# Kernel tuning notes

Hardware: AMD Instinct MI355X
Metric: run time of the kernel (lower is better)

Reference implementation:

```python
import jax, jax.numpy as jnp
import numpy as np

NUM_HEADS = 16

def _rope(t, cos, sin):
    # t: [B,H,T,hd]; cos/sin: [T,half]
    half = t.shape[-1] // 2
    t1, t2 = t[..., :half], t[..., half:]
    return jnp.concatenate((t1 * cos - t2 * sin, t1 * sin + t2 * cos), axis=-1)

def setup_inputs() -> dict:
    key = jax.random.key(0)
    ks = jax.random.split(key, 5)
    B, T, D = 2, 2048, 2048
    s = 0.02
    return {
        'x': jax.random.normal(ks[0], (B, T, D), jnp.float32),
        'w_qkv': jax.random.normal(ks[1], (3 * D, D), jnp.float32) * s,
        'b_qkv': jax.random.normal(ks[2], (3 * D,), jnp.float32) * s,
        'w_out': jax.random.normal(ks[3], (D, D), jnp.float32) * s,
        'b_out': jax.random.normal(ks[4], (D,), jnp.float32) * s,
    }

def reference(x, w_qkv, b_qkv, w_out, b_out):
    B, T, D = x.shape
    H = NUM_HEADS
    hd = D // H
    half = hd // 2
    # fused QKV projection (torch Linear: x @ W^T + b)
    qkv = (x @ w_qkv.T + b_qkv).reshape(B, T, H, 3, hd)
    q, k, v = qkv[..., 0, :], qkv[..., 1, :], qkv[..., 2, :]
    q, k, v = (jnp.transpose(t, (0, 2, 1, 3)) for t in (q, k, v))  # [B,H,T,hd]
    # RoPE frequencies (buffer computed as in __init__)
    theta = 1.0 / (10000.0 ** (jnp.arange(half, dtype=jnp.float32) / half))
    freq = jnp.arange(T, dtype=jnp.float32)[:, None] * theta[None, :]  # [T,half]
    cos, sin = jnp.cos(freq), jnp.sin(freq)
    q = _rope(q, cos, sin)
    k = _rope(k, cos, sin)
    # causal attention; NOTE: source scales by embed_dim**-0.5
    scale = D ** (-0.5)
    scores = jnp.einsum('bhqd,bhkd->bhqk', q, k) * scale
    mask = jnp.triu(jnp.full((T, T), -1e9, dtype=scores.dtype), k=1)
    weights = jax.nn.softmax(scores + mask, axis=-1)
    attn = jnp.einsum('bhqk,bhkd->bhqd', weights, v)
    attn = jnp.transpose(attn, (0, 2, 1, 3)).reshape(B, T, D)
    return attn @ w_out.T + b_out
```

## Files before the change

### kernel.cpp

```cpp
#include <hip/hip_runtime.h>
#include <math.h>

#define NHEAD 16
#define TSEQ  2048
#define BATCH 2
#define DM    2048

typedef __attribute__((ext_vector_type(8))) short bf16x8;
typedef __attribute__((ext_vector_type(4))) float f32x4;

__device__ __forceinline__ short f2bf(float f) {
    unsigned u = __builtin_bit_cast(unsigned, f);
    u += 0x7fff + ((u >> 16) & 1);
    return (short)(u >> 16);
}
__device__ __forceinline__ float bf2f(short s) {
    unsigned u = ((unsigned)(unsigned short)s) << 16;
    return __builtin_bit_cast(float, u);
}
__device__ __forceinline__ void gload_lds16(const void* g, void* l) {
    __builtin_amdgcn_global_load_lds(
        (const __attribute__((address_space(1))) unsigned int*)g,
        (__attribute__((address_space(3))) unsigned int*)l, 16, 0, 0);
}

__global__ __launch_bounds__(256)
void cast_all(const float* __restrict__ x, short* __restrict__ xb,
              const float* __restrict__ wq, short* __restrict__ wqb,
              const float* __restrict__ wo, short* __restrict__ wob)
{
    int bid = blockIdx.x;
    const float* src; short* dst; int lb;
    if (bid < 4096)       { src = x;  dst = xb;  lb = bid; }
    else if (bid < 10240) { src = wq; dst = wqb; lb = bid - 4096; }
    else                  { src = wo; dst = wob; lb = bid - 10240; }
    int i = (lb * 256 + threadIdx.x) * 8;
    float4 a = *(const float4*)(src + i);
    float4 b = *(const float4*)(src + i + 4);
    bf16x8 o;
    o[0]=f2bf(a.x); o[1]=f2bf(a.y); o[2]=f2bf(a.z); o[3]=f2bf(a.w);
    o[4]=f2bf(b.x); o[5]=f2bf(b.y); o[6]=f2bf(b.z); o[7]=f2bf(b.w);
    *(bf16x8*)(dst + i) = o;
}

__global__ __launch_bounds__(256)
void gemm_qkv_rope(const short* __restrict__ A, const short* __restrict__ W,
                   const float* __restrict__ bias, short* __restrict__ qfrag,
                   short* __restrict__ kfrag, short* __restrict__ vfrag)
{
    const int K = 2048;
    __shared__ short sm[17408];
    short* As = sm;
    short* Bs = sm + 8192;
    const int tid = threadIdx.x;
    const int lane = tid & 63, w = tid >> 6;
    const int lane15 = lane & 15, quad = lane >> 4;
    const int wr = w >> 1, wc = w & 1;
    const int row0 = blockIdx.y * 128, col0 = blockIdx.x * 128;

    f32x4 acc[4][4];
    #pragma unroll
    for (int mi = 0; mi < 4; ++mi)
        #pragma unroll
        for (int ni = 0; ni < 4; ++ni)
            acc[mi][ni] = (f32x4){0.f, 0.f, 0.f, 0.f};

    for (int kt = 0; kt < K; kt += 64) {
        __syncthreads();
        #pragma unroll
        for (int i = 0; i < 4; ++i) {
            int ci = i * 256 + tid;
            int row = ci >> 3, lc = ci & 7;
            int gc = lc ^ (row & 7);
            gload_lds16(A + (size_t)(row0 + row) * K + kt + gc * 8, As + ci * 8);
            gload_lds16(W + (size_t)(col0 + row) * K + kt + gc * 8, Bs + ci * 8);
        }
        __syncthreads();
        #pragma unroll
        for (int kc = 0; kc < 2; ++kc) {
            bf16x8 af[4], bfr[4];
            #pragma unroll
            for (int mi = 0; mi < 4; ++mi) {
                int r = wr * 64 + mi * 16 + lane15;
                af[mi] = *(const bf16x8*)(As + r * 64 + ((kc * 4 + quad) ^ (r & 7)) * 8);
            }
            #pragma unroll
            for (int ni = 0; ni < 4; ++ni) {
                int r = wc * 64 + ni * 16 + lane15;
                bfr[ni] = *(const bf16x8*)(Bs + r * 64 + ((kc * 4 + quad) ^ (r & 7)) * 8);
            }
            #pragma unroll
            for (int mi = 0; mi < 4; ++mi)
                #pragma unroll
                for (int ni = 0; ni < 4; ++ni)
                    acc[mi][ni] = __builtin_amdgcn_mfma_f32_16x16x32_bf16(
                        af[mi], bfr[ni], acc[mi][ni], 0, 0, 0);
        }
    }

    const int head = col0 / 384;
    const int type = (col0 % 384) >> 7;
    const int b    = row0 >> 11;
    const int t0g  = row0 & 2047;
    const int bh   = b * NHEAD + head;

    __syncthreads();
    #pragma unroll
    for (int ni = 0; ni < 4; ++ni) {
        int d = wc * 64 + ni * 16 + lane15;
        float bv = bias[col0 + d];
        #pragma unroll
        for (int mi = 0; mi < 4; ++mi) {
            int rowb = wr * 64 + mi * 16 + quad * 4;
            #pragma unroll
            for (int r = 0; r < 4; ++r)
                sm[(rowb + r) * 136 + d] = f2bf(acc[mi][ni][r] + bv);
        }
    }
    __syncthreads();

    if (type < 2) {
        const float sc = (type == 0) ? 0.022097086912079608f : 1.0f;
        short* dst = (type == 0 ? qfrag : kfrag) + (size_t)bh * 262144;
        #pragma unroll
        for (int it = 0; it < 4; ++it) {
            int c = it * 256 + tid;
            int l15 = c & 15, q_ = (c >> 4) & 3, kc = (c >> 6) & 1, rowhi = c >> 7;
            int lrow = rowhi * 16 + l15;
            int t = t0g + lrow;
            bf16x8 a8 = *(const bf16x8*)(sm + lrow * 136 + kc * 32 + q_ * 8);
            bf16x8 b8 = *(const bf16x8*)(sm + lrow * 136 + kc * 32 + q_ * 8 + 64);
            bf16x8 oa, ob;
            #pragma unroll
            for (int j = 0; j < 8; ++j) {
                int d = kc * 32 + q_ * 8 + j;
                float trev = exp2f(-(float)d * (13.287712379549449f / 64.0f))
                             * 0.15915494309189535f;
                float ang = (float)t * trev;
                float fr = ang - floorf(ang);
                float sn, cs;
                __sincosf(fr * 6.283185307179586f, &sn, &cs);
                float va = bf2f(a8[j]), vb = bf2f(b8[j]);
                oa[j] = f2bf((va * cs - vb * sn) * sc);
                ob[j] = f2bf((va * sn + vb * cs) * sc);
            }
            size_t base = (size_t)((t0g >> 4) + rowhi) * 2048 + (q_ * 16 + l15) * 8;
            *(bf16x8*)(dst + base + kc * 512)        = oa;
            *(bf16x8*)(dst + base + kc * 512 + 1024) = ob;
        }
    } else {
        short* dst = vfrag + (size_t)bh * 262144;
        #pragma unroll
        for (int it = 0; it < 8; ++it) {
            int c = it * 256 + tid;
            int lane_ = c & 63, rest = c >> 6;
            int q_ = lane_ >> 4, l15 = lane_ & 15;
            int dt = rest & 7, kc2 = (rest >> 3) & 1, kbt = rest >> 4;
            int d = dt * 16 + l15;
            bf16x8 v;
            #pragma unroll
            for (int j = 0; j < 8; ++j)
                v[j] = sm[(kbt * 64 + kc2 * 32 + q_ * 8 + j) * 136 + d];
            *(bf16x8*)(dst + (size_t)((t0g >> 6) + kbt) * 8192
                        + dt * 1024 + kc2 * 512 + lane_ * 8) = v;
        }
    }
}

__global__ __launch_bounds__(256)
void gemm_out(const short* __restrict__ A, const short* __restrict__ W,
              const float* __restrict__ bias, float* __restrict__ Cout,
              int N, int K)
{
    __shared__ short As[128 * 64];
    __shared__ short Bs[128 * 64];
    const int tid = threadIdx.x;
    const int lane = tid & 63, w = tid >> 6;
    const int lane15 = lane & 15, quad = lane >> 4;
    const int wr = w >> 1, wc = w & 1;
    const int row0 = blockIdx.y * 128, col0 = blockIdx.x * 128;

    f32x4 acc[4][4];
    #pragma unroll
    for (int mi = 0; mi < 4; ++mi)
        #pragma unroll
        for (int ni = 0; ni < 4; ++ni)
            acc[mi][ni] = (f32x4){0.f, 0.f, 0.f, 0.f};

    for (int kt = 0; kt < K; kt += 64) {
        __syncthreads();
        #pragma unroll
        for (int i = 0; i < 4; ++i) {
            int ci = i * 256 + tid;
            int row = ci >> 3, lc = ci & 7;
            int gc = lc ^ (row & 7);
            gload_lds16(A + (size_t)(row0 + row) * K + kt + gc * 8, As + ci * 8);
            gload_lds16(W + (size_t)(col0 + row) * K + kt + gc * 8, Bs + ci * 8);
        }
        __syncthreads();
        #pragma unroll
        for (int kc = 0; kc < 2; ++kc) {
            bf16x8 af[4], bfr[4];
            #pragma unroll
            for (int mi = 0; mi < 4; ++mi) {
                int r = wr * 64 + mi * 16 + lane15;
                af[mi] = *(const bf16x8*)(As + r * 64 + ((kc * 4 + quad) ^ (r & 7)) * 8);
            }
            #pragma unroll
            for (int ni = 0; ni < 4; ++ni) {
                int r = wc * 64 + ni * 16 + lane15;
                bfr[ni] = *(const bf16x8*)(Bs + r * 64 + ((kc * 4 + quad) ^ (r & 7)) * 8);
            }
            #pragma unroll
            for (int mi = 0; mi < 4; ++mi)
                #pragma unroll
                for (int ni = 0; ni < 4; ++ni)
                    acc[mi][ni] = __builtin_amdgcn_mfma_f32_16x16x32_bf16(
                        af[mi], bfr[ni], acc[mi][ni], 0, 0, 0);
        }
    }

    #pragma unroll
    for (int mi = 0; mi < 4; ++mi)
        #pragma unroll
        for (int ni = 0; ni < 4; ++ni) {
            int col = col0 + wc * 64 + ni * 16 + lane15;
            float bv = bias[col];
            #pragma unroll
            for (int r = 0; r < 4; ++r) {
                int row = row0 + wr * 64 + mi * 16 + quad * 4 + r;
                Cout[(size_t)row * N + col] = acc[mi][ni][r] + bv;
            }
        }
}

__global__ __launch_bounds__(256)
void attn3(const short* __restrict__ qfrag, const short* __restrict__ kfrag,
           const short* __restrict__ vfrag, short* __restrict__ attnb)
{
    __shared__ short KV[2][16384];
    __shared__ short Pb[4][1152];
    const int tid = threadIdx.x;
    const int lane = tid & 63, w = tid >> 6;
    const int lane15 = lane & 15, quad = lane >> 4;
    const int g = (blockIdx.x + blockIdx.y) & 15;
    const int qb = blockIdx.z ? (15 - g) : g;
    const int h = blockIdx.y, b = blockIdx.z;
    const int bh = b * NHEAD + h;
    const int q0 = qb * 128;
    short* Pw = Pb[w];

    bf16x8 qf[2][4];
    {
        const short* qp = qfrag + (size_t)bh * 262144
                        + (size_t)(qb * 8 + w * 2) * 2048 + lane * 8;
        #pragma unroll
        for (int nq = 0; nq < 2; ++nq)
            #pragma unroll
            for (int kc = 0; kc < 4; ++kc)
                qf[nq][kc] = *(const bf16x8*)(qp + nq * 2048 + kc * 512);
    }

    f32x4 acc[8][2];
    #pragma unroll
    for (int dt = 0; dt < 8; ++dt)
        #pragma unroll
        for (int nq = 0; nq < 2; ++nq)
            acc[dt][nq] = (f32x4){0.f, 0.f, 0.f, 0.f};
    float m_s[2] = {-3e38f, -3e38f}, l_s[2] = {0.f, 0.f};

    const short* kf_src = kfrag + (size_t)bh * 262144;
    const short* vf_src = vfrag + (size_t)bh * 262144;
    const int kb_max = 2 * qb + 1;
    const int qtop = q0 + w * 32 + 31;
    const int diag0 = (q0 + w * 32) >> 6;

    #pragma unroll
    for (int i = 0; i < 4; ++i) {
        int ci = i * 256 + tid;
        gload_lds16(kf_src + ci * 8, KV[0] + ci * 8);
        gload_lds16(vf_src + ci * 8, KV[0] + 8192 + ci * 8);
    }

    for (int kb = 0; kb <= kb_max; ++kb) {
        __syncthreads();
        if (kb < kb_max) {
            const short* ks = kf_src + (size_t)(kb + 1) * 8192;
            const short* vs = vf_src + (size_t)(kb + 1) * 8192;
            short* kd = KV[(kb + 1) & 1];
            #pragma unroll
            for (int i = 0; i < 4; ++i) {
                int ci = i * 256 + tid;
                gload_lds16(ks + ci * 8, kd + ci * 8);
                gload_lds16(vs + ci * 8, kd + 8192 + ci * 8);
            }
        }
        if (kb * 64 > qtop) continue;
        const short* Ks = KV[kb & 1];
        const short* Vs = Ks + 8192;

        f32x4 st[2][4];
        #pragma unroll
        for (int nq = 0; nq < 2; ++nq)
            #pragma unroll
            for (int mi = 0; mi < 4; ++mi)
                st[nq][mi] = (f32x4){0.f, 0.f, 0.f, 0.f};
        #pragma unroll
        for (int mi = 0; mi < 4; ++mi) {
            bf16x8 kf4[4];
            #pragma unroll
            for (int kc = 0; kc < 4; ++kc)
                kf4[kc] = *(const bf16x8*)(Ks + ((mi * 4 + kc) * 64 + lane) * 8);
            #pragma unroll
            for (int kc = 0; kc < 4; ++kc)
                #pragma unroll
                for (int nq = 0; nq < 2; ++nq)
                    st[nq][mi] = __builtin_amdgcn_mfma_f32_16x16x32_bf16(
                        kf4[kc], qf[nq][kc], st[nq][mi], 0, 0, 0);
        }

        if (kb >= diag0) {
            #pragma unroll
            for (int nq = 0; nq < 2; ++nq) {
                int qg = q0 + w * 32 + nq * 16 + lane15;
                #pragma unroll
                for (int mi = 0; mi < 4; ++mi)
                    #pragma unroll
                    for (int r = 0; r < 4; ++r)
                        if (kb * 64 + mi * 16 + quad * 4 + r > qg)
                            st[nq][mi][r] = -3e38f;
            }
        }

        bf16x8 pb[2][2];
        #pragma unroll
        for (int nq = 0; nq < 2; ++nq) {
            float mt = st[nq][0][0];
            #pragma unroll
            for (int mi = 0; mi < 4; ++mi)
                #pragma unroll
                for (int r = 0; r < 4; ++r)
                    mt = fmaxf(mt, st[nq][mi][r]);
            mt = fmaxf(mt, __shfl_xor(mt, 16));
            mt = fmaxf(mt, __shfl_xor(mt, 32));
            float mn = fmaxf(m_s[nq], mt);
            float alpha = __expf(m_s[nq] - mn);
            m_s[nq] = mn;
            float sum = 0.f;
            #pragma unroll
            for (int mi = 0; mi < 4; ++mi)
                #pragma unroll
                for (int r = 0; r < 4; ++r) {
                    float p = __expf(st[nq][mi][r] - mn);
                    st[nq][mi][r] = p;
                    sum += p;
                }
            sum += __shfl_xor(sum, 16);
            sum += __shfl_xor(sum, 32);
            l_s[nq] = l_s[nq] * alpha + sum;
            #pragma unroll
            for (int dt = 0; dt < 8; ++dt) {
                acc[dt][nq][0] *= alpha; acc[dt][nq][1] *= alpha;
                acc[dt][nq][2] *= alpha; acc[dt][nq][3] *= alpha;
            }
            short* pr = Pw + lane15 * 72 + quad * 4;
            #pragma unroll
            for (int mi = 0; mi < 4; ++mi) {
                unsigned lo = (unsigned)(unsigned short)f2bf(st[nq][mi][0])
                            | ((unsigned)(unsigned short)f2bf(st[nq][mi][1]) << 16);
                unsigned hi = (unsigned)(unsigned short)f2bf(st[nq][mi][2])
                            | ((unsigned)(unsigned short)f2bf(st[nq][mi][3]) << 16);
                *(unsigned*)(pr + mi * 16)     = lo;
                *(unsigned*)(pr + mi * 16 + 2) = hi;
            }
            __asm__ volatile("s_waitcnt lgkmcnt(0)" ::: "memory");
            #pragma unroll
            for (int kc2 = 0; kc2 < 2; ++kc2)
                pb[nq][kc2] = *(const bf16x8*)(Pw + lane15 * 72 + kc2 * 32 + quad * 8);
            __asm__ volatile("s_waitcnt lgkmcnt(0)" ::: "memory");
        }

        #pragma unroll
        for (int dt = 0; dt < 8; ++dt)
            #pragma unroll
            for (int kc2 = 0; kc2 < 2; ++kc2) {
                bf16x8 vf = *(const bf16x8*)(Vs + ((dt * 2 + kc2) * 64 + lane) * 8);
                #pragma unroll
                for (int nq = 0; nq < 2; ++nq)
                    acc[dt][nq] = __builtin_amdgcn_mfma_f32_16x16x32_bf16(
                        vf, pb[nq][kc2], acc[dt][nq], 0, 0, 0);
            }
    }

    __syncthreads();
    short* Eb = KV[0];
    #pragma unroll
    for (int nq = 0; nq < 2; ++nq) {
        float inv = 1.f / l_s[nq];
        int qrow = w * 32 + nq * 16 + lane15;
        #pragma unroll
        for (int dt = 0; dt < 8; ++dt) {
            unsigned lo = (unsigned)(unsigned short)f2bf(acc[dt][nq][0] * inv)
                        | ((unsigned)(unsigned short)f2bf(acc[dt][nq][1] * inv) << 16);
            unsigned hi = (unsigned)(unsigned short)f2bf(acc[dt][nq][2] * inv)
                        | ((unsigned)(unsigned short)f2bf(acc[dt][nq][3] * inv) << 16);
            *(unsigned*)(Eb + qrow * 136 + dt * 16 + quad * 4)     = lo;
            *(unsigned*)(Eb + qrow * 136 + dt * 16 + quad * 4 + 2) = hi;
        }
    }
    __syncthreads();
    {
        int r = tid >> 1, half = tid & 1;
        short* orow = attnb + (size_t)(b * TSEQ + q0 + r) * DM + h * 128 + half * 64;
        #pragma unroll
        for (int i = 0; i < 8; ++i)
            *(bf16x8*)(orow + i * 8) =
                *(const bf16x8*)(Eb + r * 136 + half * 64 + i * 8);
    }
}

extern "C" void kernel_launch(void* const* d_in, const int* in_sizes, int n_in,
                              void* d_out, int out_size, void* d_ws, size_t ws_size,
                              hipStream_t stream)
{
    const float* x     = (const float*)d_in[0];
    const float* w_qkv = (const float*)d_in[1];
    const float* b_qkv = (const float*)d_in[2];
    const float* w_out = (const float*)d_in[3];
    const float* b_out = (const float*)d_in[4];
    float* out = (float*)d_out;

    char* ws = (char*)d_ws;
    short* xb    = (short*)(ws);
    short* wqkvb = (short*)(ws + 16777216);
    short* woutb = (short*)(ws + 41943040);
    short* qfrag = (short*)(ws + 50331648);
    short* kfrag = (short*)(ws + 67108864);
    short* vfrag = (short*)(ws + 83886080);
    short* attnb = xb;

    cast_all<<<12288, 256, 0, stream>>>(x, xb, w_qkv, wqkvb, w_out, woutb);

    {
        dim3 g2(48, 32);
        gemm_qkv_rope<<<g2, 256, 0, stream>>>(xb, wqkvb, b_qkv, qfrag, kfrag, vfrag);
    }
    {
        dim3 g2(16, NHEAD, BATCH);
        attn3<<<g2, 256, 0, stream>>>(qfrag, kfrag, vfrag, attnb);
    }
    {
        dim3 g2(16, 32);
        gemm_out<<<g2, 256, 0, stream>>>(attnb, woutb, b_out, out, 2048, 2048);
    }
}
```

Measured before the change: 381.0 us.

## Software-pipeline attention so next QK^T overlaps softmax/PV, use exp2 softmax

Restructures the attention main loop so the QK^T MFMAs for the next key block are issued right after the softmax of the current block and before its PV MFMAs. K/V DMA is moved to the end of each iteration with prefetch distance two over the double buffer. The Q scale now folds in log2(e), so softmax can use the hardware exp2 builtin instead of __expf, and the explicit lgkmcnt waits around the P round trip through LDS are dropped. The aim is to hide softmax latency behind matrix work, at the cost of more live registers (st and pbr held across phases) and an extra barrier per iteration.

```diff
diff --git a/kernel.cpp b/kernel.cpp
--- a/kernel.cpp
+++ b/kernel.cpp
@@ -120,7 +120,7 @@
     __syncthreads();
 
     if (type < 2) {
-        const float sc = (type == 0) ? 0.022097086912079608f : 1.0f;
+        const float sc = (type == 0) ? 0.031879357813f : 1.0f;
         short* dst = (type == 0 ? qfrag : kfrag) + (size_t)bh * 262144;
         #pragma unroll
         for (int it = 0; it < 4; ++it) {
@@ -235,7 +235,7 @@
 }
 
 __global__ __launch_bounds__(256)
-void attn3(const short* __restrict__ qfrag, const short* __restrict__ kfrag,
+void attn4(const short* __restrict__ qfrag, const short* __restrict__ kfrag,
            const short* __restrict__ vfrag, short* __restrict__ attnb)
 {
     __shared__ short KV[2][16384];
@@ -275,31 +275,19 @@
     const int qtop = q0 + w * 32 + 31;
     const int diag0 = (q0 + w * 32) >> 6;
 
-    #pragma unroll
-    for (int i = 0; i < 4; ++i) {
-        int ci = i * 256 + tid;
-        gload_lds16(kf_src + ci * 8, KV[0] + ci * 8);
-        gload_lds16(vf_src + ci * 8, KV[0] + 8192 + ci * 8);
-    }
-
-    for (int kb = 0; kb <= kb_max; ++kb) {
-        __syncthreads();
-        if (kb < kb_max) {
-            const short* ks = kf_src + (size_t)(kb + 1) * 8192;
-            const short* vs = vf_src + (size_t)(kb + 1) * 8192;
-            short* kd = KV[(kb + 1) & 1];
-            #pragma unroll
-            for (int i = 0; i < 4; ++i) {
-                int ci = i * 256 + tid;
-                gload_lds16(ks + ci * 8, kd + ci * 8);
-                gload_lds16(vs + ci * 8, kd + 8192 + ci * 8);
-            }
-        }
-        if (kb * 64 > qtop) continue;
-        const short* Ks = KV[kb & 1];
-        const short* Vs = Ks + 8192;
-
-        f32x4 st[2][4];
+    auto dma = [&](int kbn, short* dst) {
+        const short* ks = kf_src + (size_t)kbn * 8192;
+        const short* vs = vf_src + (size_t)kbn * 8192;
+        #pragma unroll
+        for (int i = 0; i < 4; ++i) {
+            int ci = i * 256 + tid;
+            gload_lds16(ks + ci * 8, dst + ci * 8);
+            gload_lds16(vs + ci * 8, dst + 8192 + ci * 8);
+        }
+    };
+
+    f32x4 st[2][4];
+    auto qk = [&](const short* Ks) {
         #pragma unroll
         for (int nq = 0; nq < 2; ++nq)
             #pragma unroll
@@ -318,78 +306,101 @@
                     st[nq][mi] = __builtin_amdgcn_mfma_f32_16x16x32_bf16(
                         kf4[kc], qf[nq][kc], st[nq][mi], 0, 0, 0);
         }
-
-        if (kb >= diag0) {
+    };
+
+    dma(0, KV[0]);
+    __syncthreads();
+    dma(1, KV[1]);
+    qk(KV[0]);
+
+    for (int kb = 0; kb <= kb_max; ++kb) {
+        const short* Vs = KV[kb & 1] + 8192;
+        const bool live = (kb * 64 <= qtop);
+        bf16x8 pbr[2][2];
+
+        if (live) {
+            if (kb >= diag0) {
+                #pragma unroll
+                for (int nq = 0; nq < 2; ++nq) {
+                    int qg = q0 + w * 32 + nq * 16 + lane15;
+                    #pragma unroll
+                    for (int mi = 0; mi < 4; ++mi)
+                        #pragma unroll
+                        for (int r = 0; r < 4; ++r)
+                            if (kb * 64 + mi * 16 + quad * 4 + r > qg)
+                                st[nq][mi][r] = -3e38f;
+                }
+            }
             #pragma unroll
             for (int nq = 0; nq < 2; ++nq) {
-                int qg = q0 + w * 32 + nq * 16 + lane15;
+                float mt = st[nq][0][0];
                 #pragma unroll
                 for (int mi = 0; mi < 4; ++mi)
                     #pragma unroll
                     for (int r = 0; r < 4; ++r)
-                        if (kb * 64 + mi * 16 + quad * 4 + r > qg)
-                            st[nq][mi][r] = -3e38f;
-            }
-        }
-
-        bf16x8 pb[2][2];
-        #pragma unroll
-        for (int nq = 0; nq < 2; ++nq) {
-            float mt = st[nq][0][0];
-            #pragma unroll
-            for (int mi = 0; mi < 4; ++mi)
-                #pragma unroll
-                for (int r = 0; r < 4; ++r)
-                    mt = fmaxf(mt, st[nq][mi][r]);
-            mt = fmaxf(mt, __shfl_xor(mt, 16));
-            mt = fmaxf(mt, __shfl_xor(mt, 32));
-            float mn = fmaxf(m_s[nq], mt);
-            float alpha = __expf(m_s[nq] - mn);
-            m_s[nq] = mn;
-            float sum = 0.f;
-            #pragma unroll
-            for (int mi = 0; mi < 4; ++mi)
-                #pragma unroll
-                for (int r = 0; r < 4; ++r) {
-                    float p = __expf(st[nq][mi][r] - mn);
-                    st[nq][mi][r] = p;
-                    sum += p;
+                        mt = fmaxf(mt, st[nq][mi][r]);
+                mt = fmaxf(mt, __shfl_xor(mt, 16));
+                mt = fmaxf(mt, __shfl_xor(mt, 32));
+                float mn = fmaxf(m_s[nq], mt);
+                float alpha = __builtin_amdgcn_exp2f(m_s[nq] - mn);
+                m_s[nq] = mn;
+                float sum = 0.f;
+                #pragma unroll
+                for (int mi = 0; mi < 4; ++mi)
+                    #pragma unroll
+                    for (int r = 0; r < 4; ++r) {
+                        float p = __builtin_amdgcn_exp2f(st[nq][mi][r] - mn);
+                        st[nq][mi][r] = p;
+                        sum += p;
+                    }
+                sum += __shfl_xor(sum, 16);
+                sum += __shfl_xor(sum, 32);
+                l_s[nq] = l_s[nq] * alpha + sum;
+                #pragma unroll
+                for (int dt = 0; dt < 8; ++dt) {
+                    acc[dt][nq][0] *= alpha; acc[dt][nq][1] *= alpha;
+                    acc[dt][nq][2] *= alpha; acc[dt][nq][3] *= alpha;
                 }
-            sum += __shfl_xor(sum, 16);
-            sum += __shfl_xor(sum, 32);
-            l_s[nq] = l_s[nq] * alpha + sum;
-            #pragma unroll
-            for (int dt = 0; dt < 8; ++dt) {
-                acc[dt][nq][0] *= alpha; acc[dt][nq][1] *= alpha;
-                acc[dt][nq][2] *= alpha; acc[dt][nq][3] *= alpha;
-            }
-            short* pr = Pw + lane15 * 72 + quad * 4;
-            #pragma unroll
-            for (int mi = 0; mi < 4; ++mi) {
-                unsigned lo = (unsigned)(unsigned short)f2bf(st[nq][mi][0])
-                            | ((unsigned)(unsigned short)f2bf(st[nq][mi][1]) << 16);
-                unsigned hi = (unsigned)(unsigned short)f2bf(st[nq][mi][2])
-                            | ((unsigned)(unsigned short)f2bf(st[nq][mi][3]) << 16);
-                *(unsigned*)(pr + mi * 16)     = lo;
-                *(unsigned*)(pr + mi * 16 + 2) = hi;
-            }
-            __asm__ volatile("s_waitcnt lgkmcnt(0)" ::: "memory");
-            #pragma unroll
-            for (int kc2 = 0; kc2 < 2; ++kc2)
-                pb[nq][kc2] = *(const bf16x8*)(Pw + lane15 * 72 + kc2 * 32 + quad * 8);
-            __asm__ volatile("s_waitcnt lgkmcnt(0)" ::: "memory");
-        }
-
-        #pragma unroll
-        for (int dt = 0; dt < 8; ++dt)
-            #pragma unroll
-            for (int kc2 = 0; kc2 < 2; ++kc2) {
-                bf16x8 vf = *(const bf16x8*)(Vs + ((dt * 2 + kc2) * 64 + lane) * 8);
-                #pragma unroll
-                for (int nq = 0; nq < 2; ++nq)
-                    acc[dt][nq] = __builtin_amdgcn_mfma_f32_16x16x32_bf16(
-                        vf, pb[nq][kc2], acc[dt][nq], 0, 0, 0);
-            }
+                short* pr = Pw + lane15 * 72 + quad * 4;
+                #pragma unroll
+                for (int mi = 0; mi < 4; ++mi) {
+                    unsigned lo = (unsigned)(unsigned short)f2bf(st[nq][mi][0])
+                                | ((unsigned)(unsigned short)f2bf(st[nq][mi][1]) << 16);
+                    unsigned hi = (unsigned)(unsigned short)f2bf(st[nq][mi][2])
+                                | ((unsigned)(unsigned short)f2bf(st[nq][mi][3]) << 16);
+                    *(unsigned*)(pr + mi * 16)     = lo;
+                    *(unsigned*)(pr + mi * 16 + 2) = hi;
+                }
+                #pragma unroll
+                for (int kc2 = 0; kc2 < 2; ++kc2)
+                    pbr[nq][kc2] = *(const bf16x8*)
+                        (Pw + lane15 * 72 + kc2 * 32 + quad * 8);
+            }
+        }
+
+        if (kb < kb_max) {
+            __syncthreads();
+            if ((kb + 1) * 64 <= qtop)
+                qk(KV[(kb + 1) & 1]);
+        }
+
+        if (live) {
+            #pragma unroll
+            for (int dt = 0; dt < 8; ++dt)
+                #pragma unroll
+                for (int kc2 = 0; kc2 < 2; ++kc2) {
+                    bf16x8 vf = *(const bf16x8*)(Vs + ((dt * 2 + kc2) * 64 + lane) * 8);
+                    #pragma unroll
+                    for (int nq = 0; nq < 2; ++nq)
+                        acc[dt][nq] = __builtin_amdgcn_mfma_f32_16x16x32_bf16(
+                            vf, pbr[nq][kc2], acc[dt][nq], 0, 0, 0);
+                }
+        }
+
+        if (kb + 2 <= kb_max) {
+            __syncthreads();
+            dma(kb + 2, KV[kb & 1]);
+        }
     }
 
     __syncthreads();
@@ -447,7 +458,7 @@
     }
     {
         dim3 g2(16, NHEAD, BATCH);
-        attn3<<<g2, 256, 0, stream>>>(qfrag, kfrag, vfrag, attnb);
+        attn4<<<g2, 256, 0, stream>>>(qfrag, kfrag, vfrag, attnb);
     }
     {
         dim3 g2(16, 32);
```

After: 454.8 us. 1.19x slower.

## Shrink attention query tile to 64 rows with single-buffered KV and exp2 softmax

Applied to the files above, without the earlier changes.

Rewrites the attention kernel to give each block 64 queries (16 per wave) instead of 128, which doubles the grid to 32x16x2 and removes the per-wave causal skip logic. K/V staging moves from a double-buffered prefetch to a single buffer loaded each iteration, so load latency is no longer overlapped with compute. The log2(e) factor is folded into the Q scale so softmax can use the native exp2. The P tile now goes through LDS with an XOR swizzle in place of padding. Occupancy rises from the smaller LDS and register footprint, but each K/V tile is reused by half as many queries and the loads are exposed.

```diff
diff --git a/kernel.cpp b/kernel.cpp
--- a/kernel.cpp
+++ b/kernel.cpp
@@ -120,7 +120,7 @@
     __syncthreads();
 
     if (type < 2) {
-        const float sc = (type == 0) ? 0.022097086912079608f : 1.0f;
+        const float sc = (type == 0) ? 0.031879357813f : 1.0f;
         short* dst = (type == 0 ? qfrag : kfrag) + (size_t)bh * 262144;
         #pragma unroll
         for (int it = 0; it < 4; ++it) {
@@ -235,76 +235,54 @@
 }
 
 __global__ __launch_bounds__(256)
-void attn3(const short* __restrict__ qfrag, const short* __restrict__ kfrag,
+void attn5(const short* __restrict__ qfrag, const short* __restrict__ kfrag,
            const short* __restrict__ vfrag, short* __restrict__ attnb)
 {
-    __shared__ short KV[2][16384];
-    __shared__ short Pb[4][1152];
+    __shared__ short KV[16384];
+    __shared__ short Pb[4][1024];
     const int tid = threadIdx.x;
     const int lane = tid & 63, w = tid >> 6;
     const int lane15 = lane & 15, quad = lane >> 4;
-    const int g = (blockIdx.x + blockIdx.y) & 15;
-    const int qb = blockIdx.z ? (15 - g) : g;
+    const int g = (blockIdx.x + blockIdx.y) & 31;
+    const int qb = blockIdx.z ? (31 - g) : g;
     const int h = blockIdx.y, b = blockIdx.z;
     const int bh = b * NHEAD + h;
-    const int q0 = qb * 128;
+    const int q0 = qb * 64;
     short* Pw = Pb[w];
-
-    bf16x8 qf[2][4];
+    short* Ks = KV;
+    short* Vs = KV + 8192;
+
+    bf16x8 qf[4];
     {
         const short* qp = qfrag + (size_t)bh * 262144
-                        + (size_t)(qb * 8 + w * 2) * 2048 + lane * 8;
-        #pragma unroll
-        for (int nq = 0; nq < 2; ++nq)
-            #pragma unroll
-            for (int kc = 0; kc < 4; ++kc)
-                qf[nq][kc] = *(const bf16x8*)(qp + nq * 2048 + kc * 512);
-    }
-
-    f32x4 acc[8][2];
+                        + (size_t)(qb * 4 + w) * 2048 + lane * 8;
+        #pragma unroll
+        for (int kc = 0; kc < 4; ++kc)
+            qf[kc] = *(const bf16x8*)(qp + kc * 512);
+    }
+
+    f32x4 acc[8];
     #pragma unroll
-    for (int dt = 0; dt < 8; ++dt)
-        #pragma unroll
-        for (int nq = 0; nq < 2; ++nq)
-            acc[dt][nq] = (f32x4){0.f, 0.f, 0.f, 0.f};
-    float m_s[2] = {-3e38f, -3e38f}, l_s[2] = {0.f, 0.f};
+    for (int dt = 0; dt < 8; ++dt) acc[dt] = (f32x4){0.f, 0.f, 0.f, 0.f};
+    float m_s = -3e38f, l_s = 0.f;
 
     const short* kf_src = kfrag + (size_t)bh * 262144;
     const short* vf_src = vfrag + (size_t)bh * 262144;
-    const int kb_max = 2 * qb + 1;
-    const int qtop = q0 + w * 32 + 31;
-    const int diag0 = (q0 + w * 32) >> 6;
-
-    #pragma unroll
-    for (int i = 0; i < 4; ++i) {
-        int ci = i * 256 + tid;
-        gload_lds16(kf_src + ci * 8, KV[0] + ci * 8);
-        gload_lds16(vf_src + ci * 8, KV[0] + 8192 + ci * 8);
-    }
-
-    for (int kb = 0; kb <= kb_max; ++kb) {
+    const int qg = q0 + w * 16 + lane15;
+
+    for (int kb = 0; kb <= qb; ++kb) {
+        if (kb) __syncthreads();
+        #pragma unroll
+        for (int i = 0; i < 4; ++i) {
+            int ci = i * 256 + tid;
+            gload_lds16(kf_src + (size_t)kb * 8192 + ci * 8, Ks + ci * 8);
+            gload_lds16(vf_src + (size_t)kb * 8192 + ci * 8, Vs + ci * 8);
+        }
         __syncthreads();
-        if (kb < kb_max) {
-            const short* ks = kf_src + (size_t)(kb + 1) * 8192;
-            const short* vs = vf_src + (size_t)(kb + 1) * 8192;
-            short* kd = KV[(kb + 1) & 1];
-            #pragma unroll
-            for (int i = 0; i < 4; ++i) {
-                int ci = i * 256 + tid;
-                gload_lds16(ks + ci * 8, kd + ci * 8);
-                gload_lds16(vs + ci * 8, kd + 8192 + ci * 8);
-            }
-        }
-        if (kb * 64 > qtop) continue;
-        const short* Ks = KV[kb & 1];
-        const short* Vs = Ks + 8192;
-
-        f32x4 st[2][4];
-        #pragma unroll
-        for (int nq = 0; nq < 2; ++nq)
-            #pragma unroll
-            for (int mi = 0; mi < 4; ++mi)
-                st[nq][mi] = (f32x4){0.f, 0.f, 0.f, 0.f};
+
+        f32x4 st[4];
+        #pragma unroll
+        for (int mi = 0; mi < 4; ++mi) st[mi] = (f32x4){0.f, 0.f, 0.f, 0.f};
         #pragma unroll
         for (int mi = 0; mi < 4; ++mi) {
             bf16x8 kf4[4];
@@ -313,109 +291,97 @@
                 kf4[kc] = *(const bf16x8*)(Ks + ((mi * 4 + kc) * 64 + lane) * 8);
             #pragma unroll
             for (int kc = 0; kc < 4; ++kc)
-                #pragma unroll
-                for (int nq = 0; nq < 2; ++nq)
-                    st[nq][mi] = __builtin_amdgcn_mfma_f32_16x16x32_bf16(
-                        kf4[kc], qf[nq][kc], st[nq][mi], 0, 0, 0);
-        }
-
-        if (kb >= diag0) {
-            #pragma unroll
-            for (int nq = 0; nq < 2; ++nq) {
-                int qg = q0 + w * 32 + nq * 16 + lane15;
-                #pragma unroll
-                for (int mi = 0; mi < 4; ++mi)
-                    #pragma unroll
-                    for (int r = 0; r < 4; ++r)
-                        if (kb * 64 + mi * 16 + quad * 4 + r > qg)
-                            st[nq][mi][r] = -3e38f;
-            }
-        }
-
-        bf16x8 pb[2][2];
-        #pragma unroll
-        for (int nq = 0; nq < 2; ++nq) {
-            float mt = st[nq][0][0];
+                st[mi] = __builtin_amdgcn_mfma_f32_16x16x32_bf16(
+                    kf4[kc], qf[kc], st[mi], 0, 0, 0);
+        }
+
+        if (kb == qb) {
             #pragma unroll
             for (int mi = 0; mi < 4; ++mi)
                 #pragma unroll
                 for (int r = 0; r < 4; ++r)
-                    mt = fmaxf(mt, st[nq][mi][r]);
-            mt = fmaxf(mt, __shfl_xor(mt, 16));
-            mt = fmaxf(mt, __shfl_xor(mt, 32));
-            float mn = fmaxf(m_s[nq], mt);
-            float alpha = __expf(m_s[nq] - mn);
-            m_s[nq] = mn;
-            float sum = 0.f;
-            #pragma unroll
-            for (int mi = 0; mi < 4; ++mi)
-                #pragma unroll
-                for (int r = 0; r < 4; ++r) {
-                    float p = __expf(st[nq][mi][r] - mn);
-                    st[nq][mi][r] = p;
-                    sum += p;
-                }
-            sum += __shfl_xor(sum, 16);
-            sum += __shfl_xor(sum, 32);
-            l_s[nq] = l_s[nq] * alpha + sum;
-            #pragma unroll
-            for (int dt = 0; dt < 8; ++dt) {
-                acc[dt][nq][0] *= alpha; acc[dt][nq][1] *= alpha;
-                acc[dt][nq][2] *= alpha; acc[dt][nq][3] *= alpha;
-            }
-            short* pr = Pw + lane15 * 72 + quad * 4;
+                    if (kb * 64 + mi * 16 + quad * 4 + r > qg)
+                        st[mi][r] = -3e38f;
+        }
+
+        float mt = st[0][0];
+        #pragma unroll
+        for (int mi = 0; mi < 4; ++mi)
+            #pragma unroll
+            for (int r = 0; r < 4; ++r) mt = fmaxf(mt, st[mi][r]);
+        mt = fmaxf(mt, __shfl_xor(mt, 16));
+        mt = fmaxf(mt, __shfl_xor(mt, 32));
+        float mn = fmaxf(m_s, mt);
+        float alpha = __builtin_amdgcn_exp2f(m_s - mn);
+        m_s = mn;
+        float sum = 0.f;
+        #pragma unroll
+        for (int mi = 0; mi < 4; ++mi)
+            #pragma unroll
+            for (int r = 0; r < 4; ++r) {
+                float p = __builtin_amdgcn_exp2f(st[mi][r] - mn);
+                st[mi][r] = p;
+                sum += p;
+            }
+        sum += __shfl_xor(sum, 16);
+        sum += __shfl_xor(sum, 32);
+        l_s = l_s * alpha + sum;
+        #pragma unroll
+        for (int dt = 0; dt < 8; ++dt) {
+            acc[dt][0] *= alpha; acc[dt][1] *= alpha;
+            acc[dt][2] *= alpha; acc[dt][3] *= alpha;
+        }
+
+        {
+            short* pr = Pw + lane15 * 64 + (quad & 1) * 4;
             #pragma unroll
             for (int mi = 0; mi < 4; ++mi) {
-                unsigned lo = (unsigned)(unsigned short)f2bf(st[nq][mi][0])
-                            | ((unsigned)(unsigned short)f2bf(st[nq][mi][1]) << 16);
-                unsigned hi = (unsigned)(unsigned short)f2bf(st[nq][mi][2])
-                            | ((unsigned)(unsigned short)f2bf(st[nq][mi][3]) << 16);
-                *(unsigned*)(pr + mi * 16)     = lo;
-                *(unsigned*)(pr + mi * 16 + 2) = hi;
-            }
-            __asm__ volatile("s_waitcnt lgkmcnt(0)" ::: "memory");
-            #pragma unroll
-            for (int kc2 = 0; kc2 < 2; ++kc2)
-                pb[nq][kc2] = *(const bf16x8*)(Pw + lane15 * 72 + kc2 * 32 + quad * 8);
-            __asm__ volatile("s_waitcnt lgkmcnt(0)" ::: "memory");
-        }
+                unsigned lo = (unsigned)(unsigned short)f2bf(st[mi][0])
+                            | ((unsigned)(unsigned short)f2bf(st[mi][1]) << 16);
+                unsigned hi = (unsigned)(unsigned short)f2bf(st[mi][2])
+                            | ((unsigned)(unsigned short)f2bf(st[mi][3]) << 16);
+                int swz = (mi * 2 + (quad >> 1)) ^ (lane15 & 7);
+                *(uint2*)(pr + swz * 8) = make_uint2(lo, hi);
+            }
+        }
+        bf16x8 pbr[2];
+        #pragma unroll
+        for (int kc2 = 0; kc2 < 2; ++kc2)
+            pbr[kc2] = *(const bf16x8*)
+                (Pw + lane15 * 64 + (((kc2 * 4 + quad) ^ (lane15 & 7)) * 8));
 
         #pragma unroll
         for (int dt = 0; dt < 8; ++dt)
             #pragma unroll
             for (int kc2 = 0; kc2 < 2; ++kc2) {
                 bf16x8 vf = *(const bf16x8*)(Vs + ((dt * 2 + kc2) * 64 + lane) * 8);
-                #pragma unroll
-                for (int nq = 0; nq < 2; ++nq)
-                    acc[dt][nq] = __builtin_amdgcn_mfma_f32_16x16x32_bf16(
-                        vf, pb[nq][kc2], acc[dt][nq], 0, 0, 0);
+                acc[dt] = __builtin_amdgcn_mfma_f32_16x16x32_bf16(
+                    vf, pbr[kc2], acc[dt], 0, 0, 0);
             }
     }
 
     __syncthreads();
-    short* Eb = KV[0];
-    #pragma unroll
-    for (int nq = 0; nq < 2; ++nq) {
-        float inv = 1.f / l_s[nq];
-        int qrow = w * 32 + nq * 16 + lane15;
+    short* Eb = KV;
+    {
+        float inv = 1.f / l_s;
+        int qrow = w * 16 + lane15;
         #pragma unroll
         for (int dt = 0; dt < 8; ++dt) {
-            unsigned lo = (unsigned)(unsigned short)f2bf(acc[dt][nq][0] * inv)
-                        | ((unsigned)(unsigned short)f2bf(acc[dt][nq][1] * inv) << 16);
-            unsigned hi = (unsigned)(unsigned short)f2bf(acc[dt][nq][2] * inv)
-                        | ((unsigned)(unsigned short)f2bf(acc[dt][nq][3] * inv) << 16);
-            *(unsigned*)(Eb + qrow * 136 + dt * 16 + quad * 4)     = lo;
-            *(unsigned*)(Eb + qrow * 136 + dt * 16 + quad * 4 + 2) = hi;
+            unsigned lo = (unsigned)(unsigned short)f2bf(acc[dt][0] * inv)
+                        | ((unsigned)(unsigned short)f2bf(acc[dt][1] * inv) << 16);
+            unsigned hi = (unsigned)(unsigned short)f2bf(acc[dt][2] * inv)
+                        | ((unsigned)(unsigned short)f2bf(acc[dt][3] * inv) << 16);
+            *(uint2*)(Eb + qrow * 136 + dt * 16 + quad * 4) = make_uint2(lo, hi);
         }
     }
     __syncthreads();
     {
-        int r = tid >> 1, half = tid & 1;
-        short* orow = attnb + (size_t)(b * TSEQ + q0 + r) * DM + h * 128 + half * 64;
-        #pragma unroll
-        for (int i = 0; i < 8; ++i)
+        int r = tid >> 2, part = tid & 3;
+        short* orow = attnb + (size_t)(b * TSEQ + q0 + r) * DM + h * 128 + part * 32;
+        #pragma unroll
+        for (int i = 0; i < 4; ++i)
             *(bf16x8*)(orow + i * 8) =
-                *(const bf16x8*)(Eb + r * 136 + half * 64 + i * 8);
+                *(const bf16x8*)(Eb + r * 136 + part * 32 + i * 8);
     }
 }
 
@@ -446,8 +412,8 @@
         gemm_qkv_rope<<<g2, 256, 0, stream>>>(xb, wqkvb, b_qkv, qfrag, kfrag, vfrag);
     }
     {
-        dim3 g2(16, NHEAD, BATCH);
-        attn3<<<g2, 256, 0, stream>>>(qfrag, kfrag, vfrag, attnb);
+        dim3 g2(32, NHEAD, BATCH);
+        attn5<<<g2, 256, 0, stream>>>(qfrag, kfrag, vfrag, attnb);
     }
     {
         dim3 g2(16, 32);
```

New measurement: 390.0 us. +2.4%, slower.
